# Kernel optimization log

Measured on AMD Instinct MI355X. Metric: run time of the kernel, lower is better.

Reference implementation:

```python
import jax, jax.numpy as jnp
import numpy as np

N = 100000
E = 1600000
F_DIM = 128
H_DIM = 64
K_CLUSTERS = 16
NEG_SLOPE = 0.2


def setup_inputs() -> dict:
    key = jax.random.key(0)
    ks = jax.random.split(key, 10)
    X = jax.random.normal(ks[0], (N, F_DIM), dtype=jnp.float32)
    ei_feat = jax.random.randint(ks[1], (2, E), 0, N, dtype=jnp.int64)
    batch = jnp.zeros((N,), dtype=jnp.int64)
    # GATv2Conv layer 1 params (heads=1): lin_l, lin_r [F,H], att [H], bias [H]
    s1 = 1.0 / np.sqrt(F_DIM)
    W1l = jax.random.uniform(ks[2], (F_DIM, H_DIM), jnp.float32, -s1, s1)
    W1r = jax.random.uniform(ks[3], (F_DIM, H_DIM), jnp.float32, -s1, s1)
    a1 = jax.random.uniform(ks[4], (H_DIM,), jnp.float32, -1/np.sqrt(H_DIM), 1/np.sqrt(H_DIM))
    b1 = jnp.zeros((H_DIM,), jnp.float32)
    # layer 2: [H,K]
    s2 = 1.0 / np.sqrt(H_DIM)
    W2l = jax.random.uniform(ks[5], (H_DIM, K_CLUSTERS), jnp.float32, -s2, s2)
    W2r = jax.random.uniform(ks[6], (H_DIM, K_CLUSTERS), jnp.float32, -s2, s2)
    a2 = jax.random.uniform(ks[7], (K_CLUSTERS,), jnp.float32, -1/np.sqrt(K_CLUSTERS), 1/np.sqrt(K_CLUSTERS))
    b2 = jnp.zeros((K_CLUSTERS,), jnp.float32)
    return {"X": X, "ei_feat": ei_feat, "batch": batch,
            "W1l": W1l, "W1r": W1r, "a1": a1, "b1": b1,
            "W2l": W2l, "W2r": W2r, "a2": a2, "b2": b2}


def gatv2_conv(x, src, dst, Wl, Wr, a, b, n_nodes):
    # GATv2 (heads=1): e_ij = a^T LeakyReLU(Wl x_j + Wr x_i); softmax over j->i; out_i = sum alpha * Wl x_j
    xl = x @ Wl            # [N,H] source transform
    xr = x @ Wr            # [N,H] target transform
    e = jax.nn.leaky_relu(xl[src] + xr[dst], NEG_SLOPE) @ a   # [E']
    m = jax.ops.segment_max(e, dst, num_segments=n_nodes)      # stable softmax per target
    w = jnp.exp(e - m[dst])
    denom = jax.ops.segment_sum(w, dst, num_segments=n_nodes)
    alpha = w / denom[dst]  # every node has a self-loop, so denom > 0
    out = jax.ops.segment_sum(alpha[:, None] * xl[src], dst, num_segments=n_nodes)
    return out + b


def reference(X, ei_feat, batch, W1l, W1r, a1, b1, W2l, W2r, a2, b2):
    loop = jnp.arange(N, dtype=ei_feat.dtype)
    src = jnp.concatenate([ei_feat[0], loop])  # add_self_loops=True (PyG default)
    dst = jnp.concatenate([ei_feat[1], loop])
    h = jax.nn.elu(gatv2_conv(X, src, dst, W1l, W1r, a1, b1, N))
    z = gatv2_conv(h, src, dst, W2l, W2r, a2, b2, N)
    return jax.nn.softmax(z, axis=1)
```

## Files before the change

### kernel.cpp

```cpp
#include <hip/hip_runtime.h>
#include <stdint.h>

#define F_DIM 128
#define H_DIM 64
#define K_DIM 16
#define BUK_SH 8
#define NCH 256

typedef _Float16 half2v __attribute__((ext_vector_type(2)));
typedef _Float16 half4 __attribute__((ext_vector_type(4)));
typedef _Float16 f16x8 __attribute__((ext_vector_type(8)));
typedef float f32x4 __attribute__((ext_vector_type(4)));

__global__ __launch_bounds__(256) void k_hist(const int* __restrict__ dst,
                                              int* __restrict__ hist,
                                              int E, int CH, int NBUK) {
    __shared__ int h[512];
    int t = threadIdx.x, c = blockIdx.x;
    for (int i = t; i < NBUK; i += 256) h[i] = 0;
    __syncthreads();
    int s = c * CH, e = min(s + CH, E);
    for (int i = s + t; i < e; i += 256) atomicAdd(&h[dst[i] >> BUK_SH], 1);
    __syncthreads();
    for (int i = t; i < NBUK; i += 256) hist[i * NCH + c] = h[i];
}

__global__ __launch_bounds__(256) void k_scanBkt(int* __restrict__ hist,
                                                 int* __restrict__ bktTot) {
    __shared__ int sh[256];
    int b = blockIdx.x, t = threadIdx.x;
    int v = hist[b * NCH + t];
    sh[t] = v;
    __syncthreads();
    for (int off = 1; off < 256; off <<= 1) {
        int x = (t >= off) ? sh[t - off] : 0;
        __syncthreads();
        sh[t] += x;
        __syncthreads();
    }
    hist[b * NCH + t] = sh[t] - v;
    if (t == 255) bktTot[b] = sh[255];
}

__global__ __launch_bounds__(256) void k_scanTot(const int* __restrict__ bktTot,
                                                 int* __restrict__ bktBase, int NBUK) {
    __shared__ int sh[256];
    int t = threadIdx.x;
    int i0 = 2 * t, i1 = 2 * t + 1;
    int v0 = (i0 < NBUK) ? bktTot[i0] : 0;
    int v1 = (i1 < NBUK) ? bktTot[i1] : 0;
    int s = v0 + v1;
    sh[t] = s;
    __syncthreads();
    for (int off = 1; off < 256; off <<= 1) {
        int x = (t >= off) ? sh[t - off] : 0;
        __syncthreads();
        sh[t] += x;
        __syncthreads();
    }
    int excl = sh[t] - s;
    if (i0 < NBUK) bktBase[i0] = excl;
    if (i1 < NBUK) bktBase[i1] = excl + v0;
    if (t == 255) bktBase[NBUK] = sh[255];
}

__global__ __launch_bounds__(256) void k_scatter(const int* __restrict__ src,
                                                 const int* __restrict__ dst,
                                                 const int* __restrict__ hist,
                                                 const int* __restrict__ bktBase,
                                                 uint32_t* __restrict__ binned,
                                                 int E, int CH, int NBUK) {
    __shared__ int ctr[512];
    int t = threadIdx.x, c = blockIdx.x;
    for (int i = t; i < NBUK; i += 256) ctr[i] = bktBase[i] + hist[i * NCH + c];
    __syncthreads();
    int s = c * CH, e = min(s + CH, E);
    for (int i = s + t; i < e; i += 256) {
        int d = dst[i];
        int pos = atomicAdd(&ctr[d >> BUK_SH], 1);
        binned[pos] = (uint32_t)src[i] | ((uint32_t)(d & 255) << 20);
    }
}

__global__ __launch_bounds__(256) void k_fine2(const uint32_t* __restrict__ binned,
                                               const int* __restrict__ bktBase,
                                               int* __restrict__ rowptr,
                                               int* __restrict__ col, int N) {
    __shared__ int h[256], sc[256], slotL[256];
    int b = blockIdx.x, t = threadIdx.x;
    int n0 = b << BUK_SH;
    int s = bktBase[b], e = bktBase[b + 1];
    h[t] = 0;
    __syncthreads();
    for (int i = s + t; i < e; i += 256) atomicAdd(&h[binned[i] >> 20], 1);
    __syncthreads();
    int v = h[t];
    sc[t] = v;
    __syncthreads();
    for (int off = 1; off < 256; off <<= 1) {
        int x = (t >= off) ? sc[t - off] : 0;
        __syncthreads();
        sc[t] += x;
        __syncthreads();
    }
    int excl = sc[t] - v;
    int n = n0 + t;
    int rowbase = s + n0;
    if (n < N) {
        int rp = rowbase + excl + t;
        rowptr[n] = rp;
        col[rp] = n;
        slotL[t] = rp + 1;
        if (n == N - 1) rowptr[N] = rp + v + 1;
    }
    __syncthreads();
    for (int i = s + t; i < e; i += 256) {
        uint32_t p = binned[i];
        int pos = atomicAdd(&slotL[p >> 20], 1);
        col[pos] = (int)(p & 0xFFFFFu);
    }
}

__global__ __launch_bounds__(256) void k_gemm1m(
        const float* __restrict__ X,
        const float* __restrict__ W1l, const float* __restrict__ W1r,
        _Float16* __restrict__ xlh, _Float16* __restrict__ xrh, int N) {
    __shared__ _Float16 Ws[16384];
    __shared__ _Float16 Xs[128 * 136];
    int t = threadIdx.x;
    int n0 = blockIdx.x * 128;
    int validRows = N - n0; if (validRows > 128) validRows = 128;
    for (int i = t; i < 4096; i += 256) {
        int k = i >> 5, c4 = (i & 31) << 2;
        float4 v = (c4 < 64) ? *(const float4*)&W1l[k * 64 + c4]
                             : *(const float4*)&W1r[k * 64 + (c4 - 64)];
        int s = k >> 5, q = (k >> 3) & 3, j = k & 7;
        float vv[4] = {v.x, v.y, v.z, v.w};
#pragma unroll
        for (int u = 0; u < 4; ++u) {
            int C = c4 + u, c = C >> 4, n = C & 15;
            Ws[(((c * 4 + s) * 4 + q) * 16 + n) * 8 + j] = (_Float16)vv[u];
        }
    }
    for (int i = t; i < 4096; i += 256) {
        int r = i >> 5, c4 = (i & 31) << 2;
        float4 v = {0.f, 0.f, 0.f, 0.f};
        if (r < validRows) v = *(const float4*)&X[(long)(n0 + r) * 128 + c4];
        half4 hv;
        hv.x = (_Float16)v.x; hv.y = (_Float16)v.y;
        hv.z = (_Float16)v.z; hv.w = (_Float16)v.w;
        *(half4*)&Xs[r * 136 + c4] = hv;
    }
    __syncthreads();
    int w = t >> 6, lane = t & 63;
    int m = lane & 15, q = lane >> 4;
    f32x4 acc[2][8];
#pragma unroll
    for (int a = 0; a < 2; ++a)
#pragma unroll
        for (int c = 0; c < 8; ++c) acc[a][c] = (f32x4){0.f, 0.f, 0.f, 0.f};
#pragma unroll
    for (int s = 0; s < 4; ++s) {
        f16x8 a0 = *(const f16x8*)&Xs[(w * 32 + m) * 136 + s * 32 + q * 8];
        f16x8 a1 = *(const f16x8*)&Xs[(w * 32 + 16 + m) * 136 + s * 32 + q * 8];
#pragma unroll
        for (int c = 0; c < 8; ++c) {
            f16x8 b = *(const f16x8*)&Ws[(((c * 4 + s) * 4 + q) * 16 + m) * 8];
            acc[0][c] = __builtin_amdgcn_mfma_f32_16x16x32_f16(a0, b, acc[0][c], 0, 0, 0);
            acc[1][c] = __builtin_amdgcn_mfma_f32_16x16x32_f16(a1, b, acc[1][c], 0, 0, 0);
        }
    }
#pragma unroll
    for (int sub = 0; sub < 2; ++sub)
#pragma unroll
    for (int c = 0; c < 8; ++c)
#pragma unroll
    for (int r = 0; r < 4; ++r) {
        int gn = n0 + w * 32 + sub * 16 + q * 4 + r;
        if (gn < N) {
            int C = c * 16 + m;
            _Float16 v = (_Float16)acc[sub][c][r];
            if (C < 64) xlh[(long)gn * 64 + C] = v;
            else        xrh[(long)gn * 64 + (C - 64)] = v;
        }
    }
}

__global__ __launch_bounds__(256) void k_gemm2m(
        const _Float16* __restrict__ Hm,
        const float* __restrict__ W2l, const float* __restrict__ W2r,
        _Float16* __restrict__ xlh, _Float16* __restrict__ xrh, int N) {
    __shared__ _Float16 Ws2[2048];
    __shared__ _Float16 Hs[256 * 72];
    int t = threadIdx.x;
    int n0 = blockIdx.x * 256;
    int validRows = N - n0; if (validRows > 256) validRows = 256;
    for (int i = t; i < 512; i += 256) {
        int k = i >> 3, c4 = (i & 7) << 2;
        float4 v = (c4 < 16) ? *(const float4*)&W2l[k * 16 + c4]
                             : *(const float4*)&W2r[k * 16 + (c4 - 16)];
        int s = k >> 5, q = (k >> 3) & 3, j = k & 7;
        float vv[4] = {v.x, v.y, v.z, v.w};
#pragma unroll
        for (int u = 0; u < 4; ++u) {
            int C = c4 + u, c = C >> 4, n = C & 15;
            Ws2[(((c * 2 + s) * 4 + q) * 16 + n) * 8 + j] = (_Float16)vv[u];
        }
    }
    for (int i = t; i < 2048; i += 256) {
        int r = i >> 3, c8 = (i & 7) << 3;
        f16x8 v = {0, 0, 0, 0, 0, 0, 0, 0};
        if (r < validRows) v = *(const f16x8*)&Hm[(long)(n0 + r) * 64 + c8];
        *(f16x8*)&Hs[r * 72 + c8] = v;
    }
    __syncthreads();
    int w = t >> 6, lane = t & 63;
    int m = lane & 15, q = lane >> 4;
    f32x4 acc[4][2];
#pragma unroll
    for (int a = 0; a < 4; ++a)
#pragma unroll
        for (int c = 0; c < 2; ++c) acc[a][c] = (f32x4){0.f, 0.f, 0.f, 0.f};
#pragma unroll
    for (int s = 0; s < 2; ++s) {
        f16x8 a[4];
#pragma unroll
        for (int sub = 0; sub < 4; ++sub)
            a[sub] = *(const f16x8*)&Hs[(w * 64 + sub * 16 + m) * 72 + s * 32 + q * 8];
#pragma unroll
        for (int c = 0; c < 2; ++c) {
            f16x8 b = *(const f16x8*)&Ws2[(((c * 2 + s) * 4 + q) * 16 + m) * 8];
#pragma unroll
            for (int sub = 0; sub < 4; ++sub)
                acc[sub][c] = __builtin_amdgcn_mfma_f32_16x16x32_f16(a[sub], b, acc[sub][c], 0, 0, 0);
        }
    }
#pragma unroll
    for (int sub = 0; sub < 4; ++sub)
#pragma unroll
    for (int c = 0; c < 2; ++c)
#pragma unroll
    for (int r = 0; r < 4; ++r) {
        int gn = n0 + w * 64 + sub * 16 + q * 4 + r;
        if (gn < N) {
            int C = c * 16 + m;
            _Float16 v = (_Float16)acc[sub][c][r];
            if (C < 16) xlh[(long)gn * 16 + C] = v;
            else        xrh[(long)gn * 16 + (C - 16)] = v;
        }
    }
}

__global__ void k_att1(const f16x8* __restrict__ xlh, const f16x8* __restrict__ xrh,
                       const float* __restrict__ a1, const float* __restrict__ b1,
                       const int* __restrict__ rowptr, const int* __restrict__ col,
                       f16x8* __restrict__ hout, int N) {
    int n = (int)((blockIdx.x * (unsigned)blockDim.x + threadIdx.x) >> 6);
    int lane = threadIdx.x & 63;
    if (n >= N) return;
    int q = lane & 7;
    int g = lane >> 3;
    float4 af0 = ((const float4*)a1)[q * 2 + 0];
    float4 af1 = ((const float4*)a1)[q * 2 + 1];
    half2v a01 = {(_Float16)af0.x, (_Float16)af0.y};
    half2v a23 = {(_Float16)af0.z, (_Float16)af0.w};
    half2v a45 = {(_Float16)af1.x, (_Float16)af1.y};
    half2v a67 = {(_Float16)af1.z, (_Float16)af1.w};
    f16x8 xrv = xrh[(long)n * 8 + q];
    int jb = rowptr[n], je = rowptr[n + 1];
    float l = 0.f;
    float o[8] = {0.f, 0.f, 0.f, 0.f, 0.f, 0.f, 0.f, 0.f};
    int j = jb + g;
    for (; j + 8 < je; j += 16) {
        int s0 = col[j], s1 = col[j + 8];
        f16x8 xh0 = xlh[(long)s0 * 8 + q];
        f16x8 xh1 = xlh[(long)s1 * 8 + q];
        f16x8 t0 = xh0 + xrv, t1 = xh1 + xrv;
        f16x8 u0 = __builtin_elementwise_max(t0, t0 * (_Float16)0.2f);
        f16x8 u1 = __builtin_elementwise_max(t1, t1 * (_Float16)0.2f);
        half2v u0a = {u0[0], u0[1]}, u0b = {u0[2], u0[3]}, u0c = {u0[4], u0[5]}, u0d = {u0[6], u0[7]};
        half2v u1a = {u1[0], u1[1]}, u1b = {u1[2], u1[3]}, u1c = {u1[4], u1[5]}, u1d = {u1[6], u1[7]};
        float e0 = __builtin_amdgcn_fdot2(u0a, a01,
                    __builtin_amdgcn_fdot2(u0b, a23,
                     __builtin_amdgcn_fdot2(u0c, a45,
                      __builtin_amdgcn_fdot2(u0d, a67, 0.f, false), false), false), false);
        float e1 = __builtin_amdgcn_fdot2(u1a, a01,
                    __builtin_amdgcn_fdot2(u1b, a23,
                     __builtin_amdgcn_fdot2(u1c, a45,
                      __builtin_amdgcn_fdot2(u1d, a67, 0.f, false), false), false), false);
#pragma unroll
        for (int off = 1; off < 8; off <<= 1) {
            e0 += __shfl_xor(e0, off, 8);
            e1 += __shfl_xor(e1, off, 8);
        }
        float c0 = __expf(e0), c1 = __expf(e1);
        l += c0 + c1;
#pragma unroll
        for (int i = 0; i < 8; ++i)
            o[i] = fmaf(c0, (float)xh0[i], fmaf(c1, (float)xh1[i], o[i]));
    }
    for (; j < je; j += 8) {
        int s = col[j];
        f16x8 xh = xlh[(long)s * 8 + q];
        f16x8 t = xh + xrv;
        f16x8 u = __builtin_elementwise_max(t, t * (_Float16)0.2f);
        half2v ua = {u[0], u[1]}, ub = {u[2], u[3]}, uc = {u[4], u[5]}, ud = {u[6], u[7]};
        float e = __builtin_amdgcn_fdot2(ua, a01,
                   __builtin_amdgcn_fdot2(ub, a23,
                    __builtin_amdgcn_fdot2(uc, a45,
                     __builtin_amdgcn_fdot2(ud, a67, 0.f, false), false), false), false);
#pragma unroll
        for (int off = 1; off < 8; off <<= 1) e += __shfl_xor(e, off, 8);
        float c = __expf(e);
        l += c;
#pragma unroll
        for (int i = 0; i < 8; ++i) o[i] = fmaf(c, (float)xh[i], o[i]);
    }
#pragma unroll
    for (int off = 8; off <= 32; off <<= 1) {
        l += __shfl_xor(l, off);
#pragma unroll
        for (int i = 0; i < 8; ++i) o[i] += __shfl_xor(o[i], off);
    }
    if (g == 0) {
        float4 bv0 = ((const float4*)b1)[q * 2 + 0];
        float4 bv1 = ((const float4*)b1)[q * 2 + 1];
        float bb[8] = {bv0.x, bv0.y, bv0.z, bv0.w, bv1.x, bv1.y, bv1.z, bv1.w};
        float rl = 1.f / l;
        f16x8 hv;
#pragma unroll
        for (int i = 0; i < 8; ++i) {
            float h = o[i] * rl + bb[i];
            h = (h > 0.f) ? h : (__expf(h) - 1.f);
            hv[i] = (_Float16)h;
        }
        hout[(long)n * 8 + q] = hv;
    }
}

__global__ void k_att2(const half4* __restrict__ xlh, const half4* __restrict__ xrh,
                       const float* __restrict__ a2, const float* __restrict__ b2v,
                       const int* __restrict__ rowptr, const int* __restrict__ col,
                       float* __restrict__ out, int N) {
    int n = (int)((blockIdx.x * (unsigned)blockDim.x + threadIdx.x) >> 6);
    int lane = threadIdx.x & 63;
    if (n >= N) return;
    int q = lane & 3;
    int g = lane >> 2;
    float4 af = ((const float4*)a2)[q];
    half2v alo = {(_Float16)af.x, (_Float16)af.y};
    half2v ahi = {(_Float16)af.z, (_Float16)af.w};
    half4 xrv = xrh[(long)n * 4 + q];
    int jb = rowptr[n], je = rowptr[n + 1];
    float l = 0.f;
    float4 o = {0.f, 0.f, 0.f, 0.f};
    for (int j = jb + g; j < je; j += 16) {
        int s = col[j];
        half4 xh = xlh[(long)s * 4 + q];
        half4 t = xh + xrv;
        half4 u = __builtin_elementwise_max(t, t * (_Float16)0.2f);
        half2v ulo = {u.x, u.y}, uhi = {u.z, u.w};
        float e = __builtin_amdgcn_fdot2(ulo, alo,
                   __builtin_amdgcn_fdot2(uhi, ahi, 0.f, false), false);
        e += __shfl_xor(e, 1, 4);
        e += __shfl_xor(e, 2, 4);
        float c = __expf(e);
        l += c;
        o.x = fmaf(c, (float)xh.x, o.x);
        o.y = fmaf(c, (float)xh.y, o.y);
        o.z = fmaf(c, (float)xh.z, o.z);
        o.w = fmaf(c, (float)xh.w, o.w);
    }
#pragma unroll
    for (int off = 4; off <= 32; off <<= 1) {
        l   += __shfl_xor(l, off);
        o.x += __shfl_xor(o.x, off);
        o.y += __shfl_xor(o.y, off);
        o.z += __shfl_xor(o.z, off);
        o.w += __shfl_xor(o.w, off);
    }
    if (g == 0) {
        float4 bv = ((const float4*)b2v)[q];
        float rl = 1.f / l;
        float4 z;
        z.x = o.x * rl + bv.x;
        z.y = o.y * rl + bv.y;
        z.z = o.z * rl + bv.z;
        z.w = o.w * rl + bv.w;
        float mx = fmaxf(fmaxf(z.x, z.y), fmaxf(z.z, z.w));
        mx = fmaxf(mx, __shfl_xor(mx, 1, 4));
        mx = fmaxf(mx, __shfl_xor(mx, 2, 4));
        float4 ez;
        ez.x = __expf(z.x - mx); ez.y = __expf(z.y - mx);
        ez.z = __expf(z.z - mx); ez.w = __expf(z.w - mx);
        float ss = ez.x + ez.y + ez.z + ez.w;
        ss += __shfl_xor(ss, 1, 4);
        ss += __shfl_xor(ss, 2, 4);
        float rs = 1.f / ss;
        ez.x *= rs; ez.y *= rs; ez.z *= rs; ez.w *= rs;
        ((float4*)out)[(long)n * 4 + q] = ez;
    }
}

extern "C" void kernel_launch(void* const* d_in, const int* in_sizes, int n_in,
                              void* d_out, int out_size, void* d_ws, size_t ws_size,
                              hipStream_t stream) {
    const float* X   = (const float*)d_in[0];
    const int*   ei  = (const int*)d_in[1];
    const float* W1l = (const float*)d_in[3];
    const float* W1r = (const float*)d_in[4];
    const float* a1  = (const float*)d_in[5];
    const float* b1  = (const float*)d_in[6];
    const float* W2l = (const float*)d_in[7];
    const float* W2r = (const float*)d_in[8];
    const float* a2  = (const float*)d_in[9];
    const float* b2  = (const float*)d_in[10];

    int N = in_sizes[0] / F_DIM;
    int E = in_sizes[1] / 2;
    int M = E + N;
    int NBUK = (N + 255) >> BUK_SH;
    int NH = NBUK * NCH;
    int CH = (E + NCH - 1) / NCH;
    const int* srcv = ei;
    const int* dstv = ei + E;

    char* w = (char*)d_ws;
    size_t off = 0;
    auto alloc = [&](size_t bytes) -> char* {
        char* p = w + off;
        off = (off + bytes + 255) & ~(size_t)255;
        return p;
    };
    int* rowptr  = (int*)alloc((size_t)(N + 1) * sizeof(int));
    int* hist    = (int*)alloc((size_t)NH * sizeof(int));
    int* bktTot  = (int*)alloc((size_t)NBUK * sizeof(int));
    int* bktBase = (int*)alloc((size_t)(NBUK + 1) * sizeof(int));
    int* col     = (int*)alloc((size_t)M * sizeof(int));
    uint32_t* binned = (uint32_t*)alloc((size_t)E * sizeof(uint32_t));
    _Float16* xl1h = (_Float16*)alloc((size_t)N * H_DIM * 2);
    _Float16* xr1h = (_Float16*)alloc((size_t)N * H_DIM * 2);
    _Float16* h1h  = (_Float16*)alloc((size_t)N * H_DIM * 2);
    _Float16* xl2h = (_Float16*)alloc((size_t)N * K_DIM * 2);
    _Float16* xr2h = (_Float16*)alloc((size_t)N * K_DIM * 2);

    k_hist<<<NCH, 256, 0, stream>>>(dstv, hist, E, CH, NBUK);
    k_scanBkt<<<NBUK, 256, 0, stream>>>(hist, bktTot);
    k_scanTot<<<1, 256, 0, stream>>>(bktTot, bktBase, NBUK);
    k_scatter<<<NCH, 256, 0, stream>>>(srcv, dstv, hist, bktBase, binned, E, CH, NBUK);
    k_fine2<<<NBUK, 256, 0, stream>>>(binned, bktBase, rowptr, col, N);

    int g1Blocks = (N + 127) / 128;
    k_gemm1m<<<g1Blocks, 256, 0, stream>>>(X, W1l, W1r, xl1h, xr1h, N);
    int nodeBlocks = (N + 3) / 4;
    k_att1<<<nodeBlocks, 256, 0, stream>>>((const f16x8*)xl1h, (const f16x8*)xr1h,
                                           a1, b1, rowptr, col, (f16x8*)h1h, N);
    int g2Blocks = (N + 255) / 256;
    k_gemm2m<<<g2Blocks, 256, 0, stream>>>(h1h, W2l, W2r, xl2h, xr2h, N);
    k_att2<<<nodeBlocks, 256, 0, stream>>>((const half4*)xl2h, (const half4*)xr2h,
                                           a2, b2, rowptr, col, (float*)d_out, N);
}
```

Before: 290.3 us.

## Drop CSR fine sort; aggregate attention per 128-node bucket with LDS atomics

Removes the fine per-node sorting kernel and the rowptr/col CSR. Both attention layers now process the coarse-binned edges of each 128-node bucket directly and accumulate the softmax numerators and denominators in shared memory with float atomics. Bucket size drops from 256 to 128 nodes, with scan and shared-array sizes adjusted. This saves a kernel and a pass over the edges, but every edge now does many LDS atomic adds, and blocks get uneven work. The per-node max subtraction was already absent, and a redundant scalar store loop remains in the h output.

After: 1.119 ms. 285% more time.

```diff
diff --git a/kernel.cpp b/kernel.cpp
--- a/kernel.cpp
+++ b/kernel.cpp
@@ -4,7 +4,8 @@
 #define F_DIM 128
 #define H_DIM 64
 #define K_DIM 16
-#define BUK_SH 8
+#define BUK_SH 7
+#define BN 128
 #define NCH 256
 
 typedef _Float16 half2v __attribute__((ext_vector_type(2)));
@@ -15,7 +16,7 @@
 __global__ __launch_bounds__(256) void k_hist(const int* __restrict__ dst,
                                               int* __restrict__ hist,
                                               int E, int CH, int NBUK) {
-    __shared__ int h[512];
+    __shared__ int h[1024];
     int t = threadIdx.x, c = blockIdx.x;
     for (int i = t; i < NBUK; i += 256) h[i] = 0;
     __syncthreads();
@@ -46,10 +47,12 @@
                                                  int* __restrict__ bktBase, int NBUK) {
     __shared__ int sh[256];
     int t = threadIdx.x;
-    int i0 = 2 * t, i1 = 2 * t + 1;
-    int v0 = (i0 < NBUK) ? bktTot[i0] : 0;
-    int v1 = (i1 < NBUK) ? bktTot[i1] : 0;
-    int s = v0 + v1;
+    int base = t * 4;
+    int v0 = (base + 0 < NBUK) ? bktTot[base + 0] : 0;
+    int v1 = (base + 1 < NBUK) ? bktTot[base + 1] : 0;
+    int v2 = (base + 2 < NBUK) ? bktTot[base + 2] : 0;
+    int v3 = (base + 3 < NBUK) ? bktTot[base + 3] : 0;
+    int s = v0 + v1 + v2 + v3;
     sh[t] = s;
     __syncthreads();
     for (int off = 1; off < 256; off <<= 1) {
@@ -59,8 +62,10 @@
         __syncthreads();
     }
     int excl = sh[t] - s;
-    if (i0 < NBUK) bktBase[i0] = excl;
-    if (i1 < NBUK) bktBase[i1] = excl + v0;
+    if (base + 0 < NBUK) bktBase[base + 0] = excl;
+    if (base + 1 < NBUK) bktBase[base + 1] = excl + v0;
+    if (base + 2 < NBUK) bktBase[base + 2] = excl + v0 + v1;
+    if (base + 3 < NBUK) bktBase[base + 3] = excl + v0 + v1 + v2;
     if (t == 255) bktBase[NBUK] = sh[255];
 }
 
@@ -70,7 +75,7 @@
                                                  const int* __restrict__ bktBase,
                                                  uint32_t* __restrict__ binned,
                                                  int E, int CH, int NBUK) {
-    __shared__ int ctr[512];
+    __shared__ int ctr[1024];
     int t = threadIdx.x, c = blockIdx.x;
     for (int i = t; i < NBUK; i += 256) ctr[i] = bktBase[i] + hist[i * NCH + c];
     __syncthreads();
@@ -78,46 +83,7 @@
     for (int i = s + t; i < e; i += 256) {
         int d = dst[i];
         int pos = atomicAdd(&ctr[d >> BUK_SH], 1);
-        binned[pos] = (uint32_t)src[i] | ((uint32_t)(d & 255) << 20);
-    }
-}
-
-__global__ __launch_bounds__(256) void k_fine2(const uint32_t* __restrict__ binned,
-                                               const int* __restrict__ bktBase,
-                                               int* __restrict__ rowptr,
-                                               int* __restrict__ col, int N) {
-    __shared__ int h[256], sc[256], slotL[256];
-    int b = blockIdx.x, t = threadIdx.x;
-    int n0 = b << BUK_SH;
-    int s = bktBase[b], e = bktBase[b + 1];
-    h[t] = 0;
-    __syncthreads();
-    for (int i = s + t; i < e; i += 256) atomicAdd(&h[binned[i] >> 20], 1);
-    __syncthreads();
-    int v = h[t];
-    sc[t] = v;
-    __syncthreads();
-    for (int off = 1; off < 256; off <<= 1) {
-        int x = (t >= off) ? sc[t - off] : 0;
-        __syncthreads();
-        sc[t] += x;
-        __syncthreads();
-    }
-    int excl = sc[t] - v;
-    int n = n0 + t;
-    int rowbase = s + n0;
-    if (n < N) {
-        int rp = rowbase + excl + t;
-        rowptr[n] = rp;
-        col[rp] = n;
-        slotL[t] = rp + 1;
-        if (n == N - 1) rowptr[N] = rp + v + 1;
-    }
-    __syncthreads();
-    for (int i = s + t; i < e; i += 256) {
-        uint32_t p = binned[i];
-        int pos = atomicAdd(&slotL[p >> 20], 1);
-        col[pos] = (int)(p & 0xFFFFFu);
+        binned[pos] = (uint32_t)src[i] | ((uint32_t)(d & (BN - 1)) << 20);
     }
 }
 
@@ -251,59 +217,40 @@
     }
 }
 
-__global__ void k_att1(const f16x8* __restrict__ xlh, const f16x8* __restrict__ xrh,
-                       const float* __restrict__ a1, const float* __restrict__ b1,
-                       const int* __restrict__ rowptr, const int* __restrict__ col,
-                       f16x8* __restrict__ hout, int N) {
-    int n = (int)((blockIdx.x * (unsigned)blockDim.x + threadIdx.x) >> 6);
-    int lane = threadIdx.x & 63;
-    if (n >= N) return;
-    int q = lane & 7;
-    int g = lane >> 3;
+__global__ __launch_bounds__(256) void k_att1L(
+        const f16x8* __restrict__ xlh, const f16x8* __restrict__ xrh,
+        const float* __restrict__ a1, const float* __restrict__ b1,
+        const uint32_t* __restrict__ binned, const int* __restrict__ bktBase,
+        _Float16* __restrict__ hout, int N) {
+    __shared__ float o[BN * 65];
+    __shared__ float lAcc[BN];
+    __shared__ _Float16 xrs[BN * 64];
+    int b = blockIdx.x, t = threadIdx.x;
+    int n0 = b << BUK_SH;
+    for (int i = t; i < BN * 65; i += 256) o[i] = 0.f;
+    if (t < BN) lAcc[t] = 0.f;
+    for (int i = t; i < BN * 8; i += 256) {
+        int nd = i >> 3, q8 = i & 7;
+        f16x8 v = {0, 0, 0, 0, 0, 0, 0, 0};
+        if (n0 + nd < N) v = xrh[(long)(n0 + nd) * 8 + q8];
+        *(f16x8*)&xrs[nd * 64 + q8 * 8] = v;
+    }
+    __syncthreads();
+    int lane = t & 63, wv = t >> 6;
+    int q = lane & 7, g = lane >> 3;
     float4 af0 = ((const float4*)a1)[q * 2 + 0];
     float4 af1 = ((const float4*)a1)[q * 2 + 1];
     half2v a01 = {(_Float16)af0.x, (_Float16)af0.y};
     half2v a23 = {(_Float16)af0.z, (_Float16)af0.w};
     half2v a45 = {(_Float16)af1.x, (_Float16)af1.y};
     half2v a67 = {(_Float16)af1.z, (_Float16)af1.w};
-    f16x8 xrv = xrh[(long)n * 8 + q];
-    int jb = rowptr[n], je = rowptr[n + 1];
-    float l = 0.f;
-    float o[8] = {0.f, 0.f, 0.f, 0.f, 0.f, 0.f, 0.f, 0.f};
-    int j = jb + g;
-    for (; j + 8 < je; j += 16) {
-        int s0 = col[j], s1 = col[j + 8];
-        f16x8 xh0 = xlh[(long)s0 * 8 + q];
-        f16x8 xh1 = xlh[(long)s1 * 8 + q];
-        f16x8 t0 = xh0 + xrv, t1 = xh1 + xrv;
-        f16x8 u0 = __builtin_elementwise_max(t0, t0 * (_Float16)0.2f);
-        f16x8 u1 = __builtin_elementwise_max(t1, t1 * (_Float16)0.2f);
-        half2v u0a = {u0[0], u0[1]}, u0b = {u0[2], u0[3]}, u0c = {u0[4], u0[5]}, u0d = {u0[6], u0[7]};
-        half2v u1a = {u1[0], u1[1]}, u1b = {u1[2], u1[3]}, u1c = {u1[4], u1[5]}, u1d = {u1[6], u1[7]};
-        float e0 = __builtin_amdgcn_fdot2(u0a, a01,
-                    __builtin_amdgcn_fdot2(u0b, a23,
-                     __builtin_amdgcn_fdot2(u0c, a45,
-                      __builtin_amdgcn_fdot2(u0d, a67, 0.f, false), false), false), false);
-        float e1 = __builtin_amdgcn_fdot2(u1a, a01,
-                    __builtin_amdgcn_fdot2(u1b, a23,
-                     __builtin_amdgcn_fdot2(u1c, a45,
-                      __builtin_amdgcn_fdot2(u1d, a67, 0.f, false), false), false), false);
-#pragma unroll
-        for (int off = 1; off < 8; off <<= 1) {
-            e0 += __shfl_xor(e0, off, 8);
-            e1 += __shfl_xor(e1, off, 8);
-        }
-        float c0 = __expf(e0), c1 = __expf(e1);
-        l += c0 + c1;
-#pragma unroll
-        for (int i = 0; i < 8; ++i)
-            o[i] = fmaf(c0, (float)xh0[i], fmaf(c1, (float)xh1[i], o[i]));
-    }
-    for (; j < je; j += 8) {
-        int s = col[j];
-        f16x8 xh = xlh[(long)s * 8 + q];
-        f16x8 t = xh + xrv;
-        f16x8 u = __builtin_elementwise_max(t, t * (_Float16)0.2f);
+    for (int idx = wv * 8 + g; idx < BN; idx += 32) {
+        int gn = n0 + idx;
+        bool valid = gn < N;
+        f16x8 xh = xlh[(long)(valid ? gn : n0) * 8 + q];
+        f16x8 xrv = *(const f16x8*)&xrs[idx * 64 + q * 8];
+        f16x8 tt = xh + xrv;
+        f16x8 u = __builtin_elementwise_max(tt, tt * (_Float16)0.2f);
         half2v ua = {u[0], u[1]}, ub = {u[2], u[3]}, uc = {u[4], u[5]}, ud = {u[6], u[7]};
         float e = __builtin_amdgcn_fdot2(ua, a01,
                    __builtin_amdgcn_fdot2(ub, a23,
@@ -311,94 +258,146 @@
                      __builtin_amdgcn_fdot2(ud, a67, 0.f, false), false), false), false);
 #pragma unroll
         for (int off = 1; off < 8; off <<= 1) e += __shfl_xor(e, off, 8);
-        float c = __expf(e);
-        l += c;
-#pragma unroll
-        for (int i = 0; i < 8; ++i) o[i] = fmaf(c, (float)xh[i], o[i]);
-    }
-#pragma unroll
-    for (int off = 8; off <= 32; off <<= 1) {
-        l += __shfl_xor(l, off);
-#pragma unroll
-        for (int i = 0; i < 8; ++i) o[i] += __shfl_xor(o[i], off);
-    }
-    if (g == 0) {
-        float4 bv0 = ((const float4*)b1)[q * 2 + 0];
-        float4 bv1 = ((const float4*)b1)[q * 2 + 1];
-        float bb[8] = {bv0.x, bv0.y, bv0.z, bv0.w, bv1.x, bv1.y, bv1.z, bv1.w};
-        float rl = 1.f / l;
-        f16x8 hv;
-#pragma unroll
-        for (int i = 0; i < 8; ++i) {
-            float h = o[i] * rl + bb[i];
+        float c = valid ? __expf(e) : 0.f;
+#pragma unroll
+        for (int k = 0; k < 8; ++k)
+            atomicAdd(&o[idx * 65 + q * 8 + k], c * (float)xh[k]);
+        if (q == 0) atomicAdd(&lAcc[idx], c);
+    }
+    int s = bktBase[b], e_end = bktBase[b + 1];
+    for (int i = s + wv * 8; i < e_end; i += 32) {
+        int ie = i + g;
+        bool valid = ie < e_end;
+        uint32_t p = binned[valid ? ie : (e_end - 1)];
+        int src = (int)(p & 0xFFFFFu);
+        int nd = (int)(p >> 20) & (BN - 1);
+        f16x8 xh = xlh[(long)src * 8 + q];
+        f16x8 xrv = *(const f16x8*)&xrs[nd * 64 + q * 8];
+        f16x8 tt = xh + xrv;
+        f16x8 u = __builtin_elementwise_max(tt, tt * (_Float16)0.2f);
+        half2v ua = {u[0], u[1]}, ub = {u[2], u[3]}, uc = {u[4], u[5]}, ud = {u[6], u[7]};
+        float e = __builtin_amdgcn_fdot2(ua, a01,
+                   __builtin_amdgcn_fdot2(ub, a23,
+                    __builtin_amdgcn_fdot2(uc, a45,
+                     __builtin_amdgcn_fdot2(ud, a67, 0.f, false), false), false), false);
+#pragma unroll
+        for (int off = 1; off < 8; off <<= 1) e += __shfl_xor(e, off, 8);
+        float c = valid ? __expf(e) : 0.f;
+#pragma unroll
+        for (int k = 0; k < 8; ++k)
+            atomicAdd(&o[nd * 65 + q * 8 + k], c * (float)xh[k]);
+        if (q == 0) atomicAdd(&lAcc[nd], c);
+    }
+    __syncthreads();
+    int nd = t >> 1, hf = t & 1;
+    int gn = n0 + nd;
+    if (gn < N) {
+        float rl = 1.f / lAcc[nd];
+        _Float16 hv[32];
+#pragma unroll
+        for (int d = 0; d < 32; ++d) {
+            int dim = hf * 32 + d;
+            float h = o[nd * 65 + dim] * rl + b1[dim];
             h = (h > 0.f) ? h : (__expf(h) - 1.f);
-            hv[i] = (_Float16)h;
-        }
-        hout[(long)n * 8 + q] = hv;
-    }
-}
-
-__global__ void k_att2(const half4* __restrict__ xlh, const half4* __restrict__ xrh,
-                       const float* __restrict__ a2, const float* __restrict__ b2v,
-                       const int* __restrict__ rowptr, const int* __restrict__ col,
-                       float* __restrict__ out, int N) {
-    int n = (int)((blockIdx.x * (unsigned)blockDim.x + threadIdx.x) >> 6);
-    int lane = threadIdx.x & 63;
-    if (n >= N) return;
-    int q = lane & 3;
-    int g = lane >> 2;
+            hv[d] = (_Float16)h;
+        }
+#pragma unroll
+        for (int j = 0; j < 4; ++j)
+            hout[(long)gn * 64 + hf * 32 + j * 8 + 0] = hv[j * 8];
+#pragma unroll
+        for (int j = 0; j < 4; ++j)
+            *(f16x8*)&hout[(long)gn * 64 + hf * 32 + j * 8] = *(f16x8*)&hv[j * 8];
+    }
+}
+
+__global__ __launch_bounds__(256) void k_att2L(
+        const half4* __restrict__ xlh, const half4* __restrict__ xrh,
+        const float* __restrict__ a2, const float* __restrict__ b2v,
+        const uint32_t* __restrict__ binned, const int* __restrict__ bktBase,
+        float* __restrict__ out, int N) {
+    __shared__ float o2[BN * 19];
+    __shared__ float l2[BN];
+    __shared__ _Float16 xr2s[BN * 16];
+    int b = blockIdx.x, t = threadIdx.x;
+    int n0 = b << BUK_SH;
+    for (int i = t; i < BN * 19; i += 256) o2[i] = 0.f;
+    if (t < BN) l2[t] = 0.f;
+    for (int i = t; i < BN * 4; i += 256) {
+        int nd = i >> 2, q4 = i & 3;
+        half4 v = {0, 0, 0, 0};
+        if (n0 + nd < N) v = xrh[(long)(n0 + nd) * 4 + q4];
+        *(half4*)&xr2s[nd * 16 + q4 * 4] = v;
+    }
+    __syncthreads();
+    int lane = t & 63, wv = t >> 6;
+    int q = lane & 3, g = lane >> 2;
     float4 af = ((const float4*)a2)[q];
     half2v alo = {(_Float16)af.x, (_Float16)af.y};
     half2v ahi = {(_Float16)af.z, (_Float16)af.w};
-    half4 xrv = xrh[(long)n * 4 + q];
-    int jb = rowptr[n], je = rowptr[n + 1];
-    float l = 0.f;
-    float4 o = {0.f, 0.f, 0.f, 0.f};
-    for (int j = jb + g; j < je; j += 16) {
-        int s = col[j];
-        half4 xh = xlh[(long)s * 4 + q];
-        half4 t = xh + xrv;
-        half4 u = __builtin_elementwise_max(t, t * (_Float16)0.2f);
+    for (int idx = wv * 16 + g; idx < BN; idx += 64) {
+        int gn = n0 + idx;
+        bool valid = gn < N;
+        half4 xh = xlh[(long)(valid ? gn : n0) * 4 + q];
+        half4 xrv = *(const half4*)&xr2s[idx * 16 + q * 4];
+        half4 tt = xh + xrv;
+        half4 u = __builtin_elementwise_max(tt, tt * (_Float16)0.2f);
         half2v ulo = {u.x, u.y}, uhi = {u.z, u.w};
         float e = __builtin_amdgcn_fdot2(ulo, alo,
                    __builtin_amdgcn_fdot2(uhi, ahi, 0.f, false), false);
         e += __shfl_xor(e, 1, 4);
         e += __shfl_xor(e, 2, 4);
-        float c = __expf(e);
-        l += c;
-        o.x = fmaf(c, (float)xh.x, o.x);
-        o.y = fmaf(c, (float)xh.y, o.y);
-        o.z = fmaf(c, (float)xh.z, o.z);
-        o.w = fmaf(c, (float)xh.w, o.w);
-    }
-#pragma unroll
-    for (int off = 4; off <= 32; off <<= 1) {
-        l   += __shfl_xor(l, off);
-        o.x += __shfl_xor(o.x, off);
-        o.y += __shfl_xor(o.y, off);
-        o.z += __shfl_xor(o.z, off);
-        o.w += __shfl_xor(o.w, off);
-    }
-    if (g == 0) {
-        float4 bv = ((const float4*)b2v)[q];
-        float rl = 1.f / l;
-        float4 z;
-        z.x = o.x * rl + bv.x;
-        z.y = o.y * rl + bv.y;
-        z.z = o.z * rl + bv.z;
-        z.w = o.w * rl + bv.w;
-        float mx = fmaxf(fmaxf(z.x, z.y), fmaxf(z.z, z.w));
-        mx = fmaxf(mx, __shfl_xor(mx, 1, 4));
-        mx = fmaxf(mx, __shfl_xor(mx, 2, 4));
-        float4 ez;
-        ez.x = __expf(z.x - mx); ez.y = __expf(z.y - mx);
-        ez.z = __expf(z.z - mx); ez.w = __expf(z.w - mx);
-        float ss = ez.x + ez.y + ez.z + ez.w;
-        ss += __shfl_xor(ss, 1, 4);
-        ss += __shfl_xor(ss, 2, 4);
-        float rs = 1.f / ss;
-        ez.x *= rs; ez.y *= rs; ez.z *= rs; ez.w *= rs;
-        ((float4*)out)[(long)n * 4 + q] = ez;
+        float c = valid ? __expf(e) : 0.f;
+        atomicAdd(&o2[idx * 19 + q * 4 + 0], c * (float)xh.x);
+        atomicAdd(&o2[idx * 19 + q * 4 + 1], c * (float)xh.y);
+        atomicAdd(&o2[idx * 19 + q * 4 + 2], c * (float)xh.z);
+        atomicAdd(&o2[idx * 19 + q * 4 + 3], c * (float)xh.w);
+        if (q == 0) atomicAdd(&l2[idx], c);
+    }
+    int s = bktBase[b], e_end = bktBase[b + 1];
+    for (int i = s + wv * 16; i < e_end; i += 64) {
+        int ie = i + g;
+        bool valid = ie < e_end;
+        uint32_t p = binned[valid ? ie : (e_end - 1)];
+        int src = (int)(p & 0xFFFFFu);
+        int nd = (int)(p >> 20) & (BN - 1);
+        half4 xh = xlh[(long)src * 4 + q];
+        half4 xrv = *(const half4*)&xr2s[nd * 16 + q * 4];
+        half4 tt = xh + xrv;
+        half4 u = __builtin_elementwise_max(tt, tt * (_Float16)0.2f);
+        half2v ulo = {u.x, u.y}, uhi = {u.z, u.w};
+        float e = __builtin_amdgcn_fdot2(ulo, alo,
+                   __builtin_amdgcn_fdot2(uhi, ahi, 0.f, false), false);
+        e += __shfl_xor(e, 1, 4);
+        e += __shfl_xor(e, 2, 4);
+        float c = valid ? __expf(e) : 0.f;
+        atomicAdd(&o2[nd * 19 + q * 4 + 0], c * (float)xh.x);
+        atomicAdd(&o2[nd * 19 + q * 4 + 1], c * (float)xh.y);
+        atomicAdd(&o2[nd * 19 + q * 4 + 2], c * (float)xh.z);
+        atomicAdd(&o2[nd * 19 + q * 4 + 3], c * (float)xh.w);
+        if (q == 0) atomicAdd(&l2[nd], c);
+    }
+    __syncthreads();
+    if (t < BN) {
+        int gn = n0 + t;
+        if (gn < N) {
+            float rl = 1.f / l2[t];
+            float z[16];
+            float mx = -1e30f;
+#pragma unroll
+            for (int d = 0; d < 16; ++d) {
+                z[d] = o2[t * 19 + d] * rl + b2v[d];
+                mx = fmaxf(mx, z[d]);
+            }
+            float ss = 0.f;
+#pragma unroll
+            for (int d = 0; d < 16; ++d) { z[d] = __expf(z[d] - mx); ss += z[d]; }
+            float rs = 1.f / ss;
+#pragma unroll
+            for (int d = 0; d < 16; d += 4) {
+                float4 v = {z[d] * rs, z[d + 1] * rs, z[d + 2] * rs, z[d + 3] * rs};
+                *(float4*)&out[(long)gn * 16 + d] = v;
+            }
+        }
     }
 }
 
@@ -418,8 +417,7 @@
 
     int N = in_sizes[0] / F_DIM;
     int E = in_sizes[1] / 2;
-    int M = E + N;
-    int NBUK = (N + 255) >> BUK_SH;
+    int NBUK = (N + BN - 1) >> BUK_SH;
     int NH = NBUK * NCH;
     int CH = (E + NCH - 1) / NCH;
     const int* srcv = ei;
@@ -432,11 +430,9 @@
         off = (off + bytes + 255) & ~(size_t)255;
         return p;
     };
-    int* rowptr  = (int*)alloc((size_t)(N + 1) * sizeof(int));
     int* hist    = (int*)alloc((size_t)NH * sizeof(int));
     int* bktTot  = (int*)alloc((size_t)NBUK * sizeof(int));
     int* bktBase = (int*)alloc((size_t)(NBUK + 1) * sizeof(int));
-    int* col     = (int*)alloc((size_t)M * sizeof(int));
     uint32_t* binned = (uint32_t*)alloc((size_t)E * sizeof(uint32_t));
     _Float16* xl1h = (_Float16*)alloc((size_t)N * H_DIM * 2);
     _Float16* xr1h = (_Float16*)alloc((size_t)N * H_DIM * 2);
@@ -448,15 +444,13 @@
     k_scanBkt<<<NBUK, 256, 0, stream>>>(hist, bktTot);
     k_scanTot<<<1, 256, 0, stream>>>(bktTot, bktBase, NBUK);
     k_scatter<<<NCH, 256, 0, stream>>>(srcv, dstv, hist, bktBase, binned, E, CH, NBUK);
-    k_fine2<<<NBUK, 256, 0, stream>>>(binned, bktBase, rowptr, col, N);
 
     int g1Blocks = (N + 127) / 128;
     k_gemm1m<<<g1Blocks, 256, 0, stream>>>(X, W1l, W1r, xl1h, xr1h, N);
-    int nodeBlocks = (N + 3) / 4;
-    k_att1<<<nodeBlocks, 256, 0, stream>>>((const f16x8*)xl1h, (const f16x8*)xr1h,
-                                           a1, b1, rowptr, col, (f16x8*)h1h, N);
+    k_att1L<<<NBUK, 256, 0, stream>>>((const f16x8*)xl1h, (const f16x8*)xr1h,
+                                      a1, b1, binned, bktBase, h1h, N);
     int g2Blocks = (N + 255) / 256;
     k_gemm2m<<<g2Blocks, 256, 0, stream>>>(h1h, W2l, W2r, xl2h, xr2h, N);
-    k_att2<<<nodeBlocks, 256, 0, stream>>>((const half4*)xl2h, (const half4*)xr2h,
-                                           a2, b2, rowptr, col, (float*)d_out, N);
-}
+    k_att2L<<<NBUK, 256, 0, stream>>>((const half4*)xl2h, (const half4*)xr2h,
+                                      a2, b2, binned, bktBase, (float*)d_out, N);
+}
```
